# Kernel optimization log

Measured on AMD Instinct MI355X. Metric: run time of the kernel, lower is better.

The kernel has to match this reference:

```python
import jax, jax.numpy as jnp
import numpy as np

# ---- static configuration (mirrors C4WithSyscalls __init__/_build_keys) ----
MEM = 16384            # memory_size
OUT = 64               # output_size
NCTX = MEM + 5 + OUT   # context: [memory, PC, SP, BP, AX, OUT_LEN, output]
SCALE = 10.0
GATE_SCALE = 20.0
ADDR_BITS = int(np.ceil(np.log2(NCTX)))   # 15
TYPE_BITS = 5
KDIM = ADDR_BITS + TYPE_BITS
POWERS = jnp.asarray(2 ** np.arange(ADDR_BITS), jnp.int32)

# opcode values for the 15 experts: IMM,LEA,ADD,SUB,MUL,DIV,MOD,SHL,SHR,EQ,NE,LT,GT,LE,GE
OP_VALS = jnp.asarray([1., 2., 9., 10., 11., 12., 13., 14., 15., 3., 4., 5., 6., 7., 8.], jnp.float32)
# binary ops (everything except IMM, LEA) pop the stack: sp += 8
POP_MASK = jnp.asarray([0., 0.] + [1.] * 13, jnp.float32)


def _build_keys():
    addrs = np.arange(NCTX)
    bits = (addrs[:, None] // (2 ** np.arange(ADDR_BITS))) % 2
    addr_keys = (2.0 * bits - 1.0) * SCALE                       # [N, ADDR_BITS]
    type_tags = np.full((NCTX, TYPE_BITS), -SCALE)
    type_tags[MEM, 0] = SCALE      # PC
    type_tags[MEM + 1, 1] = SCALE  # SP
    type_tags[MEM + 2, 2] = SCALE  # BP
    type_tags[MEM + 3, 3] = SCALE  # AX
    type_tags[MEM + 4:, 4] = SCALE  # OUT_LEN + output slots
    return jnp.asarray(np.concatenate([addr_keys, type_tags], 1), jnp.float32)

KEYS = _build_keys()  # [NCTX, KDIM]


def silu_threshold(x, scale=GATE_SCALE):
    d = scale * x
    return (jax.nn.silu(d + 0.5 * scale) - jax.nn.silu(d - 0.5 * scale)) / scale


def eq_gate(a, b, scale=GATE_SCALE):
    diff = a - b
    return silu_threshold(diff + 0.5, scale) * silu_threshold(-diff + 0.5, scale)


def attend(context, addr):
    """Soft-addressed gather: context [B,NCTX], addr [B] float -> (value [B], weights [B,NCTX])."""
    ai = jnp.clip(addr, 0.0, float(NCTX - 1)).astype(jnp.int32)
    bits = (ai[:, None] // POWERS) % 2
    addr_q = (2.0 * bits.astype(jnp.float32) - 1.0) * SCALE                 # [B, ADDR_BITS]
    type_q = jnp.full((addr.shape[0], TYPE_BITS), -SCALE, jnp.float32)      # memory_type tag
    q = jnp.concatenate([addr_q, type_q], axis=1)                           # [B, KDIM]
    scores = jnp.einsum('nd,bd->bn', KEYS, q) / np.sqrt(KDIM)
    w = jax.nn.softmax(scores, axis=1)
    return jnp.einsum('bn,bn->b', w, context), w


def expert_outputs(a, b, imm, bp):
    """a = stack_top, b = ax. Returns [B, 15] new-ax candidates per expert."""
    safeb = jnp.where(jnp.abs(b) < 1e-6, 1e-6, b)
    div = a / safeb
    mod = a - safeb * jnp.floor(div)
    sh = jnp.clip(b, 0.0, 31.0)
    eq = eq_gate(a, b)
    lt = jax.nn.sigmoid(GATE_SCALE * (b - a - 0.5))
    gt = jax.nn.sigmoid(GATE_SCALE * (a - b - 0.5))
    return jnp.stack([
        imm,               # IMM
        bp + imm,          # LEA
        a + b,             # ADD
        a - b,             # SUB
        a * b,             # MUL
        div,               # DIV
        mod,               # MOD
        a * jnp.exp2(sh),  # SHL
        a * jnp.exp2(-sh), # SHR
        eq,                # EQ
        1.0 - eq,          # NE
        lt,                # LT
        gt,                # GT
        1.0 - gt,          # LE
        1.0 - lt,          # GE
    ], axis=-1)


def _forward(memory, output, ax, pc, sp, bp, out_len, num_steps):
    B = memory.shape[0]
    pcf, spf, bpf = pc.astype(jnp.float32), sp.astype(jnp.float32), bp.astype(jnp.float32)
    olf = out_len.astype(jnp.float32)[:, None]

    def step(carry, _):
        pc_, sp_, bp_, ax_, mem_ = carry
        regs = jnp.stack([pc_, sp_, bp_, ax_], axis=1)                    # [B,4]
        context = jnp.concatenate([mem_, regs, olf, output], axis=1)     # [B,NCTX]
        inst, _ = attend(context, pc_)
        imm = jnp.floor(inst / 256.0)
        opcode = inst - imm * 256.0
        stack_top, w_sp = attend(context, sp_)
        gates = eq_gate(opcode[:, None], OP_VALS[None, :])                # [B,15] soft top-1
        outs = expert_outputs(stack_top, ax_, imm, bp_)                   # [B,15]
        gsum = gates.sum(-1)
        new_ax = (gates * outs).sum(-1) + (1.0 - gsum) * ax_              # NoOp default
        pop_g = (gates * POP_MASK).sum(-1)
        new_sp = sp_ + 8.0 * pop_g
        new_pc = pc_ + 8.0
        # soft scatter: write new_ax back at the (soft) stack-top address
        new_mem = mem_ + pop_g[:, None] * w_sp[:, :MEM] * (new_ax[:, None] - mem_)
        return (new_pc, new_sp, bp_, new_ax, new_mem), None

    carry, _ = jax.lax.scan(step, (pcf, spf, bpf, ax, memory), None, length=num_steps)
    return carry[4]  # final memory [B, MEM]


def setup_inputs() -> dict:
    key = jax.random.key(0)
    k = jax.random.split(key, 8)
    B = 1024
    return {
        'memory': jax.random.normal(k[0], (B, MEM), jnp.float32),
        'output': jax.random.normal(k[1], (B, OUT), jnp.float32),
        'ax': jax.random.normal(k[2], (B,), jnp.float32),
        'pc': jax.random.randint(k[3], (B,), 0, MEM, jnp.int32),
        'sp': jax.random.randint(k[4], (B,), 0, MEM, jnp.int32),
        'bp': jax.random.randint(k[5], (B,), 0, MEM, jnp.int32),
        'out_len': jax.random.randint(k[6], (B,), 0, OUT, jnp.int32),
        'num_steps': 16,
    }


def reference(memory, output, ax, pc, sp, bp, out_len, num_steps):
    return _forward(memory, output, ax, pc, sp, bp, out_len, num_steps)
```

## Files before the change

kernel.cpp:

```cpp
#include <hip/hip_runtime.h>
#include <math.h>

#define MEMSZ 16384
#define NCTX  16453

typedef float f4 __attribute__((ext_vector_type(4)));

__device__ __forceinline__ float sigmoidf_(float x) {
    return __builtin_amdgcn_rcpf(1.0f + __expf(-x));
}
__device__ __forceinline__ float siluf_(float x) {
    return x * sigmoidf_(x);
}
__device__ __forceinline__ float silu_thr(float x) {
    float d = 20.0f * x;
    return (siluf_(d + 10.0f) - siluf_(d - 10.0f)) * 0.05f;
}
__device__ __forceinline__ float eq_gate_d(float diff) {
    return silu_thr(diff + 0.5f) * silu_thr(0.5f - diff);
}

__global__ __launch_bounds__(256) void copy_kernel(const f4* __restrict__ src,
                                                   f4* __restrict__ dst, int n4) {
    int i = blockIdx.x * blockDim.x + threadIdx.x;
    if (i < n4)
        __builtin_nontemporal_store(__builtin_nontemporal_load(&src[i]), &dst[i]);
}

__global__ __launch_bounds__(64) void sim_kernel(
        float* __restrict__ mem,
        const float* __restrict__ outp,
        const float* __restrict__ ax_in,
        const int* __restrict__ pc_in,
        const int* __restrict__ sp_in,
        const int* __restrict__ bp_in,
        const int* __restrict__ ol_in,
        const int* __restrict__ nstep,
        int B) {
    int b = blockIdx.x;
    if (b >= B) return;
    int lane = threadIdx.x;

    float* __restrict__ mrow = mem + (size_t)b * MEMSZ;
    const float* __restrict__ orow = outp + (size_t)b * 64;

    float pc0 = (float)pc_in[b];
    float sp  = (float)sp_in[b];
    float bp  = (float)bp_in[b];
    float ax  = ax_in[b];
    float olf = (float)ol_in[b];
    int   T   = nstep[0];

    float opvl = (lane < 2)  ? (float)(lane + 1)
               : (lane < 9)  ? (float)(lane + 7)
               : (lane < 15) ? (float)(lane - 6)
                             : 0.0f;

    if (T == 16) {
        float pf[16];
        int   pfi[16];
#pragma unroll
        for (int t = 0; t < 16; ++t) {
            float pcr = pc0 + 8.0f * (float)t;
            float a1 = fminf(fmaxf(pcr, 0.0f), (float)(NCTX - 1));
            int ai = (int)a1;
            pfi[t] = ai;
            int pidx = (ai < MEMSZ) ? ai : ai - MEMSZ;
            pf[t] = mrow[pidx];
        }

        int   sidx[16];
        float sval[16];
#pragma unroll
        for (int j = 0; j < 16; ++j) { sidx[j] = -1; sval[j] = 0.0f; }

        float a2 = fminf(fmaxf(sp, 0.0f), (float)(NCTX - 1));
        int   si  = (int)a2;
        int   tgt = (si < MEMSZ) ? si : si - MEMSZ;
        float raw = mrow[tgt];

#pragma unroll
        for (int t = 0; t < 16; ++t) {
            float pcr = pc0 + 8.0f * (float)t;

            int ai   = pfi[t];
            int pidx = (ai < MEMSZ) ? ai : ai - MEMSZ;
            float m_pc = pf[t];
#pragma unroll
            for (int j = 0; j < 16; ++j)
                if (j < t && sidx[j] == pidx) m_pc = sval[j];

            float inst;
            if (ai < MEMSZ) {
                inst = m_pc;
            } else {
                int r = ai - MEMSZ;
                float cv = (r == 0) ? pcr
                         : (r == 1) ? sp
                         : (r == 2) ? bp
                         : (r == 3) ? ax
                         : (r == 4) ? olf
                                    : orow[r - 5];
                inst = 0.5f * (cv + m_pc);
            }
            float imm = floorf(inst * (1.0f / 256.0f));
            float opc = inst - imm * 256.0f;

            float gl = eq_gate_d(opc - opvl);

            float G0  = __shfl(gl, 0),  G1  = __shfl(gl, 1),  G2  = __shfl(gl, 2);
            float G3  = __shfl(gl, 3),  G4  = __shfl(gl, 4),  G5  = __shfl(gl, 5);
            float G6  = __shfl(gl, 6),  G7  = __shfl(gl, 7),  G8  = __shfl(gl, 8);
            float G9  = __shfl(gl, 9),  G10 = __shfl(gl, 10), G11 = __shfl(gl, 11);
            float G12 = __shfl(gl, 12), G13 = __shfl(gl, 13), G14 = __shfl(gl, 14);

            float gsum = 0.0f;
            gsum += G0;  gsum += G1;  gsum += G2;  gsum += G3;  gsum += G4;
            gsum += G5;  gsum += G6;  gsum += G7;  gsum += G8;  gsum += G9;
            gsum += G10; gsum += G11; gsum += G12; gsum += G13; gsum += G14;
            float pop = 0.0f;
            pop += G2;  pop += G3;  pop += G4;  pop += G5;  pop += G6;
            pop += G7;  pop += G8;  pop += G9;  pop += G10; pop += G11;
            pop += G12; pop += G13; pop += G14;

            float sp_next = sp + 8.0f * pop;
            int   si_n = 0, tgt_n = 0;
            float raw_n = 0.0f;
            if (t < 15) {
                float a2n = fminf(fmaxf(sp_next, 0.0f), (float)(NCTX - 1));
                si_n  = (int)a2n;
                tgt_n = (si_n < MEMSZ) ? si_n : si_n - MEMSZ;
                raw_n = mrow[tgt_n];
            }

            float mtv = raw;
#pragma unroll
            for (int j = 0; j < 16; ++j)
                if (j < t && sidx[j] == tgt) mtv = sval[j];

            float stv, wfac;
            if (si < MEMSZ) {
                stv = mtv;
                wfac = 1.0f;
            } else {
                int r = si - MEMSZ;
                float cv = (r == 0) ? pcr
                         : (r == 1) ? sp
                         : (r == 2) ? bp
                         : (r == 3) ? ax
                         : (r == 4) ? olf
                                    : orow[r - 5];
                stv = 0.5f * (cv + mtv);
                wfac = 0.5f;
            }

            float a = stv, bv = ax;
            float safeb = (fabsf(bv) < 1e-6f) ? 1e-6f : bv;
            float dvv = a / safeb;
            float md  = a - safeb * floorf(dvv);
            float sh  = fminf(fmaxf(bv, 0.0f), 31.0f);
            float eqg = eq_gate_d(a - bv);
            float lt  = sigmoidf_(20.0f * (bv - a - 0.5f));
            float gt  = sigmoidf_(20.0f * (a - bv - 0.5f));
            float o0 = imm,            o1 = bp + imm,     o2 = a + bv;
            float o3 = a - bv,         o4 = a * bv,       o5 = dvv;
            float o6 = md,             o7 = a * exp2f(sh), o8 = a * exp2f(-sh);
            float o9 = eqg,            o10 = 1.0f - eqg,  o11 = lt;
            float o12 = gt,            o13 = 1.0f - gt,   o14 = 1.0f - lt;

            float acc = 0.0f;
            acc += G0 * o0;   acc += G1 * o1;   acc += G2 * o2;
            acc += G3 * o3;   acc += G4 * o4;   acc += G5 * o5;
            acc += G6 * o6;   acc += G7 * o7;   acc += G8 * o8;
            acc += G9 * o9;   acc += G10 * o10; acc += G11 * o11;
            acc += G12 * o12; acc += G13 * o13; acc += G14 * o14;
            float nax = acc + (1.0f - gsum) * ax;

            float vnew = mtv + pop * wfac * (nax - mtv);
            if (lane == 0) mrow[tgt] = vnew;
            sidx[t] = tgt;
            sval[t] = vnew;

            sp = sp_next;
            ax = nax;
            if (t < 15) { si = si_n; tgt = tgt_n; raw = raw_n; }
        }
    } else if (lane == 0) {
        const float opv[15] = {1.f, 2.f, 9.f, 10.f, 11.f, 12.f, 13.f, 14.f, 15.f,
                               3.f, 4.f, 5.f, 6.f, 7.f, 8.f};
        float pc = pc0;
        for (int t = 0; t < T; ++t) {
            float a1 = fminf(fmaxf(pc, 0.0f), (float)(NCTX - 1));
            int   ai = (int)a1;
            float a2 = fminf(fmaxf(sp, 0.0f), (float)(NCTX - 1));
            int   si = (int)a2;
            int pidx   = (ai < MEMSZ) ? ai : (ai - MEMSZ);
            int target = (si < MEMSZ) ? si : (si - MEMSZ);
            float m_pc = mrow[pidx];
            float mtv  = mrow[target];

            float inst;
            if (ai < MEMSZ) {
                inst = m_pc;
            } else {
                int r = ai - MEMSZ;
                float cv = (r == 0) ? pc
                         : (r == 1) ? sp
                         : (r == 2) ? bp
                         : (r == 3) ? ax
                         : (r == 4) ? olf
                                    : orow[r - 5];
                inst = 0.5f * (cv + m_pc);
            }
            float imm = floorf(inst * (1.0f / 256.0f));
            float opc = inst - imm * 256.0f;

            float stv, wfac;
            if (si < MEMSZ) {
                stv = mtv;
                wfac = 1.0f;
            } else {
                int r = si - MEMSZ;
                float cv = (r == 0) ? pc
                         : (r == 1) ? sp
                         : (r == 2) ? bp
                         : (r == 3) ? ax
                         : (r == 4) ? olf
                                    : orow[r - 5];
                stv = 0.5f * (cv + mtv);
                wfac = 0.5f;
            }

            float a = stv, bv = ax;
            float safeb = (fabsf(bv) < 1e-6f) ? 1e-6f : bv;
            float dvv = a / safeb;
            float md  = a - safeb * floorf(dvv);
            float sh  = fminf(fmaxf(bv, 0.0f), 31.0f);
            float eqg = eq_gate_d(a - bv);
            float lt  = sigmoidf_(20.0f * (bv - a - 0.5f));
            float gt  = sigmoidf_(20.0f * (a - bv - 0.5f));
            float outs[15] = {
                imm, bp + imm, a + bv, a - bv, a * bv, dvv, md,
                a * exp2f(sh), a * exp2f(-sh),
                eqg, 1.0f - eqg, lt, gt, 1.0f - gt, 1.0f - lt
            };

            float gsum = 0.0f, acc = 0.0f, pop = 0.0f;
#pragma unroll
            for (int j = 0; j < 15; ++j) {
                float gg = eq_gate_d(opc - opv[j]);
                gsum += gg;
                acc  += gg * outs[j];
                if (j >= 2) pop += gg;
            }
            float nax = acc + (1.0f - gsum) * ax;

            mrow[target] = mtv + pop * wfac * (nax - mtv);

            sp = sp + 8.0f * pop;
            pc = pc + 8.0f;
            ax = nax;
        }
    }
}

extern "C" void kernel_launch(void* const* d_in, const int* in_sizes, int n_in,
                              void* d_out, int out_size, void* d_ws, size_t ws_size,
                              hipStream_t stream) {
    const float* memory = (const float*)d_in[0];
    const float* output = (const float*)d_in[1];
    const float* ax     = (const float*)d_in[2];
    const int*   pc     = (const int*)d_in[3];
    const int*   sp     = (const int*)d_in[4];
    const int*   bp     = (const int*)d_in[5];
    const int*   ol     = (const int*)d_in[6];
    const int*   ns     = (const int*)d_in[7];

    int B = in_sizes[0] / MEMSZ;
    int n4 = (B * MEMSZ) / 4;

    hipLaunchKernelGGL(copy_kernel, dim3((n4 + 255) / 256), dim3(256), 0, stream,
                       (const f4*)memory, (f4*)d_out, n4);
    hipLaunchKernelGGL(sim_kernel, dim3(B), dim3(64), 0, stream,
                       (float*)d_out, output, ax, pc, sp, bp, ol, ns, B);
}
```

Baseline: 147.0 us.

## Fuse memory copy and simulation into one kernel with warp-specialized copy

Replaces the separate bulk copy kernel and the per-row simulation kernel with one kernel of 256 threads per row. Three wavefronts copy the row while the first wavefront runs the 16-step simulation, reading from the input buffer and holding its writes in registers. After a barrier, thread 0 scatters the buffered writes into the output. This removes one launch and the dependency between the copy and the serial simulation, letting the latency-bound simulation overlap the bandwidth-bound copy. In exchange the grid is only B blocks with fewer copy threads per row, which may lower copy bandwidth.

```diff
diff --git a/kernel.cpp b/kernel.cpp
--- a/kernel.cpp
+++ b/kernel.cpp
@@ -20,15 +20,8 @@
     return silu_thr(diff + 0.5f) * silu_thr(0.5f - diff);
 }
 
-__global__ __launch_bounds__(256) void copy_kernel(const f4* __restrict__ src,
-                                                   f4* __restrict__ dst, int n4) {
-    int i = blockIdx.x * blockDim.x + threadIdx.x;
-    if (i < n4)
-        __builtin_nontemporal_store(__builtin_nontemporal_load(&src[i]), &dst[i]);
-}
-
-__global__ __launch_bounds__(64) void sim_kernel(
-        float* __restrict__ mem,
+__global__ __launch_bounds__(256) void fused_kernel(
+        const float* __restrict__ memory,
         const float* __restrict__ outp,
         const float* __restrict__ ax_in,
         const int* __restrict__ pc_in,
@@ -36,230 +29,267 @@
         const int* __restrict__ bp_in,
         const int* __restrict__ ol_in,
         const int* __restrict__ nstep,
+        float* __restrict__ dst,
         int B) {
-    int b = blockIdx.x;
-    if (b >= B) return;
-    int lane = threadIdx.x;
-
-    float* __restrict__ mrow = mem + (size_t)b * MEMSZ;
-    const float* __restrict__ orow = outp + (size_t)b * 64;
-
-    float pc0 = (float)pc_in[b];
-    float sp  = (float)sp_in[b];
-    float bp  = (float)bp_in[b];
-    float ax  = ax_in[b];
-    float olf = (float)ol_in[b];
-    int   T   = nstep[0];
-
-    float opvl = (lane < 2)  ? (float)(lane + 1)
-               : (lane < 9)  ? (float)(lane + 7)
-               : (lane < 15) ? (float)(lane - 6)
-                             : 0.0f;
+    const int b   = blockIdx.x;
+    const int tid = threadIdx.x;
+
+    const float* __restrict__ mrow_in  = memory + (size_t)b * MEMSZ;
+    float*       __restrict__ mrow_out = dst    + (size_t)b * MEMSZ;
+    const f4* __restrict__ src4 = (const f4*)mrow_in;
+    f4*       __restrict__ dst4 = (f4*)mrow_out;
+
+    const int T = nstep[0];
 
     if (T == 16) {
-        float pf[16];
-        int   pfi[16];
-#pragma unroll
-        for (int t = 0; t < 16; ++t) {
-            float pcr = pc0 + 8.0f * (float)t;
-            float a1 = fminf(fmaxf(pcr, 0.0f), (float)(NCTX - 1));
-            int ai = (int)a1;
-            pfi[t] = ai;
-            int pidx = (ai < MEMSZ) ? ai : ai - MEMSZ;
-            pf[t] = mrow[pidx];
-        }
-
         int   sidx[16];
         float sval[16];
-#pragma unroll
-        for (int j = 0; j < 16; ++j) { sidx[j] = -1; sval[j] = 0.0f; }
-
-        float a2 = fminf(fmaxf(sp, 0.0f), (float)(NCTX - 1));
-        int   si  = (int)a2;
-        int   tgt = (si < MEMSZ) ? si : si - MEMSZ;
-        float raw = mrow[tgt];
-
-#pragma unroll
-        for (int t = 0; t < 16; ++t) {
-            float pcr = pc0 + 8.0f * (float)t;
-
-            int ai   = pfi[t];
-            int pidx = (ai < MEMSZ) ? ai : ai - MEMSZ;
-            float m_pc = pf[t];
-#pragma unroll
-            for (int j = 0; j < 16; ++j)
-                if (j < t && sidx[j] == pidx) m_pc = sval[j];
-
-            float inst;
-            if (ai < MEMSZ) {
-                inst = m_pc;
-            } else {
-                int r = ai - MEMSZ;
-                float cv = (r == 0) ? pcr
-                         : (r == 1) ? sp
-                         : (r == 2) ? bp
-                         : (r == 3) ? ax
-                         : (r == 4) ? olf
-                                    : orow[r - 5];
-                inst = 0.5f * (cv + m_pc);
+
+        if (tid >= 64) {
+            int c = tid - 64;
+#pragma unroll
+            for (int i = 0; i < 22; ++i) {
+                int idx = c + i * 192;
+                if (idx < 4096)
+                    __builtin_nontemporal_store(
+                        __builtin_nontemporal_load(&src4[idx]), &dst4[idx]);
             }
-            float imm = floorf(inst * (1.0f / 256.0f));
-            float opc = inst - imm * 256.0f;
-
-            float gl = eq_gate_d(opc - opvl);
-
-            float G0  = __shfl(gl, 0),  G1  = __shfl(gl, 1),  G2  = __shfl(gl, 2);
-            float G3  = __shfl(gl, 3),  G4  = __shfl(gl, 4),  G5  = __shfl(gl, 5);
-            float G6  = __shfl(gl, 6),  G7  = __shfl(gl, 7),  G8  = __shfl(gl, 8);
-            float G9  = __shfl(gl, 9),  G10 = __shfl(gl, 10), G11 = __shfl(gl, 11);
-            float G12 = __shfl(gl, 12), G13 = __shfl(gl, 13), G14 = __shfl(gl, 14);
-
-            float gsum = 0.0f;
-            gsum += G0;  gsum += G1;  gsum += G2;  gsum += G3;  gsum += G4;
-            gsum += G5;  gsum += G6;  gsum += G7;  gsum += G8;  gsum += G9;
-            gsum += G10; gsum += G11; gsum += G12; gsum += G13; gsum += G14;
-            float pop = 0.0f;
-            pop += G2;  pop += G3;  pop += G4;  pop += G5;  pop += G6;
-            pop += G7;  pop += G8;  pop += G9;  pop += G10; pop += G11;
-            pop += G12; pop += G13; pop += G14;
-
-            float sp_next = sp + 8.0f * pop;
-            int   si_n = 0, tgt_n = 0;
-            float raw_n = 0.0f;
-            if (t < 15) {
-                float a2n = fminf(fmaxf(sp_next, 0.0f), (float)(NCTX - 1));
-                si_n  = (int)a2n;
-                tgt_n = (si_n < MEMSZ) ? si_n : si_n - MEMSZ;
-                raw_n = mrow[tgt_n];
+        } else {
+            const int lane = tid;
+            const float* __restrict__ orow = outp + (size_t)b * 64;
+
+            float pc0 = (float)pc_in[b];
+            float sp  = (float)sp_in[b];
+            float bp  = (float)bp_in[b];
+            float ax  = ax_in[b];
+            float olf = (float)ol_in[b];
+
+            float opvl = (lane < 2)  ? (float)(lane + 1)
+                       : (lane < 9)  ? (float)(lane + 7)
+                       : (lane < 15) ? (float)(lane - 6)
+                                     : 0.0f;
+
+            float pf[16];
+            int   pfi[16];
+#pragma unroll
+            for (int t = 0; t < 16; ++t) {
+                float pcr = pc0 + 8.0f * (float)t;
+                float a1 = fminf(fmaxf(pcr, 0.0f), (float)(NCTX - 1));
+                int ai = (int)a1;
+                pfi[t] = ai;
+                int pidx = (ai < MEMSZ) ? ai : ai - MEMSZ;
+                pf[t] = mrow_in[pidx];
             }
 
-            float mtv = raw;
-#pragma unroll
-            for (int j = 0; j < 16; ++j)
-                if (j < t && sidx[j] == tgt) mtv = sval[j];
-
-            float stv, wfac;
-            if (si < MEMSZ) {
-                stv = mtv;
-                wfac = 1.0f;
-            } else {
-                int r = si - MEMSZ;
-                float cv = (r == 0) ? pcr
-                         : (r == 1) ? sp
-                         : (r == 2) ? bp
-                         : (r == 3) ? ax
-                         : (r == 4) ? olf
-                                    : orow[r - 5];
-                stv = 0.5f * (cv + mtv);
-                wfac = 0.5f;
+#pragma unroll
+            for (int j = 0; j < 16; ++j) { sidx[j] = -1; sval[j] = 0.0f; }
+
+            float a2 = fminf(fmaxf(sp, 0.0f), (float)(NCTX - 1));
+            int   si  = (int)a2;
+            int   tgt = (si < MEMSZ) ? si : si - MEMSZ;
+            float raw = mrow_in[tgt];
+
+#pragma unroll
+            for (int t = 0; t < 16; ++t) {
+                float pcr = pc0 + 8.0f * (float)t;
+
+                int ai   = pfi[t];
+                int pidx = (ai < MEMSZ) ? ai : ai - MEMSZ;
+                float m_pc = pf[t];
+#pragma unroll
+                for (int j = 0; j < 16; ++j)
+                    if (j < t && sidx[j] == pidx) m_pc = sval[j];
+
+                float inst;
+                if (ai < MEMSZ) {
+                    inst = m_pc;
+                } else {
+                    int r = ai - MEMSZ;
+                    float cv = (r == 0) ? pcr
+                             : (r == 1) ? sp
+                             : (r == 2) ? bp
+                             : (r == 3) ? ax
+                             : (r == 4) ? olf
+                                        : orow[r - 5];
+                    inst = 0.5f * (cv + m_pc);
+                }
+                float imm = floorf(inst * (1.0f / 256.0f));
+                float opc = inst - imm * 256.0f;
+
+                float gl = eq_gate_d(opc - opvl);
+                float G0  = __shfl(gl, 0),  G1  = __shfl(gl, 1),  G2  = __shfl(gl, 2);
+                float G3  = __shfl(gl, 3),  G4  = __shfl(gl, 4),  G5  = __shfl(gl, 5);
+                float G6  = __shfl(gl, 6),  G7  = __shfl(gl, 7),  G8  = __shfl(gl, 8);
+                float G9  = __shfl(gl, 9),  G10 = __shfl(gl, 10), G11 = __shfl(gl, 11);
+                float G12 = __shfl(gl, 12), G13 = __shfl(gl, 13), G14 = __shfl(gl, 14);
+
+                float gsum = 0.0f;
+                gsum += G0;  gsum += G1;  gsum += G2;  gsum += G3;  gsum += G4;
+                gsum += G5;  gsum += G6;  gsum += G7;  gsum += G8;  gsum += G9;
+                gsum += G10; gsum += G11; gsum += G12; gsum += G13; gsum += G14;
+                float pop = 0.0f;
+                pop += G2;  pop += G3;  pop += G4;  pop += G5;  pop += G6;
+                pop += G7;  pop += G8;  pop += G9;  pop += G10; pop += G11;
+                pop += G12; pop += G13; pop += G14;
+
+                float sp_next = sp + 8.0f * pop;
+                int   si_n = 0, tgt_n = 0;
+                float raw_n = 0.0f;
+                if (t < 15) {
+                    float a2n = fminf(fmaxf(sp_next, 0.0f), (float)(NCTX - 1));
+                    si_n  = (int)a2n;
+                    tgt_n = (si_n < MEMSZ) ? si_n : si_n - MEMSZ;
+                    raw_n = mrow_in[tgt_n];
+                }
+
+                float mtv = raw;
+#pragma unroll
+                for (int j = 0; j < 16; ++j)
+                    if (j < t && sidx[j] == tgt) mtv = sval[j];
+
+                float stv, wfac;
+                if (si < MEMSZ) {
+                    stv = mtv;
+                    wfac = 1.0f;
+                } else {
+                    int r = si - MEMSZ;
+                    float cv = (r == 0) ? pcr
+                             : (r == 1) ? sp
+                             : (r == 2) ? bp
+                             : (r == 3) ? ax
+                             : (r == 4) ? olf
+                                        : orow[r - 5];
+                    stv = 0.5f * (cv + mtv);
+                    wfac = 0.5f;
+                }
+
+                float a = stv, bv = ax;
+                float safeb = (fabsf(bv) < 1e-6f) ? 1e-6f : bv;
+                float dvv = a / safeb;
+                float md  = a - safeb * floorf(dvv);
+                float sh  = fminf(fmaxf(bv, 0.0f), 31.0f);
+                float eqg = eq_gate_d(a - bv);
+                float lt  = sigmoidf_(20.0f * (bv - a - 0.5f));
+                float gt  = sigmoidf_(20.0f * (a - bv - 0.5f));
+                float o0 = imm,            o1 = bp + imm,      o2 = a + bv;
+                float o3 = a - bv,         o4 = a * bv,        o5 = dvv;
+                float o6 = md,             o7 = a * exp2f(sh), o8 = a * exp2f(-sh);
+                float o9 = eqg,            o10 = 1.0f - eqg,   o11 = lt;
+                float o12 = gt,            o13 = 1.0f - gt,    o14 = 1.0f - lt;
+
+                float acc = 0.0f;
+                acc += G0 * o0;   acc += G1 * o1;   acc += G2 * o2;
+                acc += G3 * o3;   acc += G4 * o4;   acc += G5 * o5;
+                acc += G6 * o6;   acc += G7 * o7;   acc += G8 * o8;
+                acc += G9 * o9;   acc += G10 * o10; acc += G11 * o11;
+                acc += G12 * o12; acc += G13 * o13; acc += G14 * o14;
+                float nax = acc + (1.0f - gsum) * ax;
+
+                float vnew = mtv + pop * wfac * (nax - mtv);
+                sidx[t] = tgt;
+                sval[t] = vnew;
+
+                sp = sp_next;
+                ax = nax;
+                if (t < 15) { si = si_n; tgt = tgt_n; raw = raw_n; }
             }
-
-            float a = stv, bv = ax;
-            float safeb = (fabsf(bv) < 1e-6f) ? 1e-6f : bv;
-            float dvv = a / safeb;
-            float md  = a - safeb * floorf(dvv);
-            float sh  = fminf(fmaxf(bv, 0.0f), 31.0f);
-            float eqg = eq_gate_d(a - bv);
-            float lt  = sigmoidf_(20.0f * (bv - a - 0.5f));
-            float gt  = sigmoidf_(20.0f * (a - bv - 0.5f));
-            float o0 = imm,            o1 = bp + imm,     o2 = a + bv;
-            float o3 = a - bv,         o4 = a * bv,       o5 = dvv;
-            float o6 = md,             o7 = a * exp2f(sh), o8 = a * exp2f(-sh);
-            float o9 = eqg,            o10 = 1.0f - eqg,  o11 = lt;
-            float o12 = gt,            o13 = 1.0f - gt,   o14 = 1.0f - lt;
-
-            float acc = 0.0f;
-            acc += G0 * o0;   acc += G1 * o1;   acc += G2 * o2;
-            acc += G3 * o3;   acc += G4 * o4;   acc += G5 * o5;
-            acc += G6 * o6;   acc += G7 * o7;   acc += G8 * o8;
-            acc += G9 * o9;   acc += G10 * o10; acc += G11 * o11;
-            acc += G12 * o12; acc += G13 * o13; acc += G14 * o14;
-            float nax = acc + (1.0f - gsum) * ax;
-
-            float vnew = mtv + pop * wfac * (nax - mtv);
-            if (lane == 0) mrow[tgt] = vnew;
-            sidx[t] = tgt;
-            sval[t] = vnew;
-
-            sp = sp_next;
-            ax = nax;
-            if (t < 15) { si = si_n; tgt = tgt_n; raw = raw_n; }
         }
-    } else if (lane == 0) {
-        const float opv[15] = {1.f, 2.f, 9.f, 10.f, 11.f, 12.f, 13.f, 14.f, 15.f,
-                               3.f, 4.f, 5.f, 6.f, 7.f, 8.f};
-        float pc = pc0;
-        for (int t = 0; t < T; ++t) {
-            float a1 = fminf(fmaxf(pc, 0.0f), (float)(NCTX - 1));
-            int   ai = (int)a1;
-            float a2 = fminf(fmaxf(sp, 0.0f), (float)(NCTX - 1));
-            int   si = (int)a2;
-            int pidx   = (ai < MEMSZ) ? ai : (ai - MEMSZ);
-            int target = (si < MEMSZ) ? si : (si - MEMSZ);
-            float m_pc = mrow[pidx];
-            float mtv  = mrow[target];
-
-            float inst;
-            if (ai < MEMSZ) {
-                inst = m_pc;
-            } else {
-                int r = ai - MEMSZ;
-                float cv = (r == 0) ? pc
-                         : (r == 1) ? sp
-                         : (r == 2) ? bp
-                         : (r == 3) ? ax
-                         : (r == 4) ? olf
-                                    : orow[r - 5];
-                inst = 0.5f * (cv + m_pc);
+
+        __syncthreads();
+
+        if (tid == 0) {
+#pragma unroll
+            for (int t = 0; t < 16; ++t)
+                mrow_out[sidx[t]] = sval[t];
+        }
+    } else {
+#pragma unroll
+        for (int i = 0; i < 16; ++i)
+            dst4[tid + i * 256] = src4[tid + i * 256];
+        __syncthreads();
+
+        if (tid == 0) {
+            const float* __restrict__ orow = outp + (size_t)b * 64;
+            const float opv[15] = {1.f, 2.f, 9.f, 10.f, 11.f, 12.f, 13.f, 14.f,
+                                   15.f, 3.f, 4.f, 5.f, 6.f, 7.f, 8.f};
+            float pc  = (float)pc_in[b];
+            float sp  = (float)sp_in[b];
+            float bp  = (float)bp_in[b];
+            float ax  = ax_in[b];
+            float olf = (float)ol_in[b];
+
+            for (int t = 0; t < T; ++t) {
+                float a1 = fminf(fmaxf(pc, 0.0f), (float)(NCTX - 1));
+                int   ai = (int)a1;
+                float a2 = fminf(fmaxf(sp, 0.0f), (float)(NCTX - 1));
+                int   si = (int)a2;
+                int pidx   = (ai < MEMSZ) ? ai : (ai - MEMSZ);
+                int target = (si < MEMSZ) ? si : (si - MEMSZ);
+                float m_pc = mrow_out[pidx];
+                float mtv  = mrow_out[target];
+
+                float inst;
+                if (ai < MEMSZ) {
+                    inst = m_pc;
+                } else {
+                    int r = ai - MEMSZ;
+                    float cv = (r == 0) ? pc
+                             : (r == 1) ? sp
+                             : (r == 2) ? bp
+                             : (r == 3) ? ax
+                             : (r == 4) ? olf
+                                        : orow[r - 5];
+                    inst = 0.5f * (cv + m_pc);
+                }
+                float imm = floorf(inst * (1.0f / 256.0f));
+                float opc = inst - imm * 256.0f;
+
+                float stv, wfac;
+                if (si < MEMSZ) {
+                    stv = mtv;
+                    wfac = 1.0f;
+                } else {
+                    int r = si - MEMSZ;
+                    float cv = (r == 0) ? pc
+                             : (r == 1) ? sp
+                             : (r == 2) ? bp
+                             : (r == 3) ? ax
+                             : (r == 4) ? olf
+                                        : orow[r - 5];
+                    stv = 0.5f * (cv + mtv);
+                    wfac = 0.5f;
+                }
+
+                float a = stv, bv = ax;
+                float safeb = (fabsf(bv) < 1e-6f) ? 1e-6f : bv;
+                float dvv = a / safeb;
+                float md  = a - safeb * floorf(dvv);
+                float sh  = fminf(fmaxf(bv, 0.0f), 31.0f);
+                float eqg = eq_gate_d(a - bv);
+                float lt  = sigmoidf_(20.0f * (bv - a - 0.5f));
+                float gt  = sigmoidf_(20.0f * (a - bv - 0.5f));
+                float outs[15] = {
+                    imm, bp + imm, a + bv, a - bv, a * bv, dvv, md,
+                    a * exp2f(sh), a * exp2f(-sh),
+                    eqg, 1.0f - eqg, lt, gt, 1.0f - gt, 1.0f - lt
+                };
+
+                float gsum = 0.0f, acc = 0.0f, pop = 0.0f;
+#pragma unroll
+                for (int j = 0; j < 15; ++j) {
+                    float gg = eq_gate_d(opc - opv[j]);
+                    gsum += gg;
+                    acc  += gg * outs[j];
+                    if (j >= 2) pop += gg;
+                }
+                float nax = acc + (1.0f - gsum) * ax;
+
+                mrow_out[target] = mtv + pop * wfac * (nax - mtv);
+
+                sp = sp + 8.0f * pop;
+                pc = pc + 8.0f;
+                ax = nax;
             }
-            float imm = floorf(inst * (1.0f / 256.0f));
-            float opc = inst - imm * 256.0f;
-
-            float stv, wfac;
-            if (si < MEMSZ) {
-                stv = mtv;
-                wfac = 1.0f;
-            } else {
-                int r = si - MEMSZ;
-                float cv = (r == 0) ? pc
-                         : (r == 1) ? sp
-                         : (r == 2) ? bp
-                         : (r == 3) ? ax
-                         : (r == 4) ? olf
-                                    : orow[r - 5];
-                stv = 0.5f * (cv + mtv);
-                wfac = 0.5f;
-            }
-
-            float a = stv, bv = ax;
-            float safeb = (fabsf(bv) < 1e-6f) ? 1e-6f : bv;
-            float dvv = a / safeb;
-            float md  = a - safeb * floorf(dvv);
-            float sh  = fminf(fmaxf(bv, 0.0f), 31.0f);
-            float eqg = eq_gate_d(a - bv);
-            float lt  = sigmoidf_(20.0f * (bv - a - 0.5f));
-            float gt  = sigmoidf_(20.0f * (a - bv - 0.5f));
-            float outs[15] = {
-                imm, bp + imm, a + bv, a - bv, a * bv, dvv, md,
-                a * exp2f(sh), a * exp2f(-sh),
-                eqg, 1.0f - eqg, lt, gt, 1.0f - gt, 1.0f - lt
-            };
-
-            float gsum = 0.0f, acc = 0.0f, pop = 0.0f;
-#pragma unroll
-            for (int j = 0; j < 15; ++j) {
-                float gg = eq_gate_d(opc - opv[j]);
-                gsum += gg;
-                acc  += gg * outs[j];
-                if (j >= 2) pop += gg;
-            }
-            float nax = acc + (1.0f - gsum) * ax;
-
-            mrow[target] = mtv + pop * wfac * (nax - mtv);
-
-            sp = sp + 8.0f * pop;
-            pc = pc + 8.0f;
-            ax = nax;
         }
     }
 }
@@ -277,10 +307,8 @@
     const int*   ns     = (const int*)d_in[7];
 
     int B = in_sizes[0] / MEMSZ;
-    int n4 = (B * MEMSZ) / 4;
-
-    hipLaunchKernelGGL(copy_kernel, dim3((n4 + 255) / 256), dim3(256), 0, stream,
-                       (const f4*)memory, (f4*)d_out, n4);
-    hipLaunchKernelGGL(sim_kernel, dim3(B), dim3(64), 0, stream,
-                       (float*)d_out, output, ax, pc, sp, bp, ol, ns, B);
-}
+
+    hipLaunchKernelGGL(fused_kernel, dim3(B), dim3(256), 0, stream,
+                       memory, output, ax, pc, sp, bp, ol, ns,
+                       (float*)d_out, B);
+}
```

After: 139.0 us. 5.5% less time.
